# Performance work log

Measured on AMD Instinct MI355X. Metric: run time of the kernel, lower is better.

The kernel has to match this reference:

```python
import jax, jax.numpy as jnp
import numpy as np


def _sq_cdist(a, b):
    # squared Euclidean distances, [N, M]
    a2 = jnp.sum(a * a, axis=1)[:, None]
    b2 = jnp.sum(b * b, axis=1)[None, :]
    d = a2 + b2 - 2.0 * (a @ b.T)
    return jnp.maximum(d, 0.0)


def _gaussian_kernel_mean(a, b, sigmas):
    # mean over N*M of sum_k exp(-dist / (2*sigma_k))
    dist = _sq_cdist(a, b)                      # [N, M]
    beta = 1.0 / (2.0 * sigmas)                 # [K]
    s = jnp.exp(-beta[:, None, None] * dist[None, :, :])  # [K, N, M]
    return jnp.mean(jnp.sum(s, axis=0))


def setup_inputs() -> dict:
    key = jax.random.key(0)
    k1, k2 = jax.random.split(key)
    B, C, H, W = 4, 256, 32, 32
    x = jax.random.normal(k1, (B, C, H, W), dtype=jnp.float32)
    y = jax.random.normal(k2, (B, C, H, W), dtype=jnp.float32)
    sigmas = jnp.array([0.01, 0.1, 1.0, 10.0, 100.0], dtype=jnp.float32)
    return {"x": x, "y": y, "sigmas": sigmas}


def reference(x, y, sigmas):
    B, C, H, W = x.shape
    # (B,C,H,W) -> (B*H*W, C), matching flatten(2).transpose(1,2).reshape(-1,C)
    xf = jnp.transpose(x.reshape(B, C, H * W), (0, 2, 1)).reshape(-1, C)
    yf = jnp.transpose(y.reshape(B, C, H * W), (0, 2, 1)).reshape(-1, C)
    xx = _gaussian_kernel_mean(xf, xf, sigmas)
    yy = _gaussian_kernel_mean(yf, yf, sigmas)
    xy = _gaussian_kernel_mean(xf, yf, sigmas)
    return xx + yy - 2.0 * xy
```

## Files before the change

### kernel.cpp

```cpp
#include <hip/hip_runtime.h>
#include <hip/hip_bf16.h>


#define NSIG 5
#define CKS   262144
#define NBLK2 2080

typedef __attribute__((ext_vector_type(8))) short short8;
typedef __attribute__((ext_vector_type(4))) float floatx4;

__global__ __launch_bounds__(256) void prep_kernel(const float* __restrict__ x,
                                                   const float* __restrict__ y,
                                                   ushort* __restrict__ Zc,
                                                   float* __restrict__ norms) {
    const int bid = blockIdx.x;
    const int t = threadIdx.x;
    const int s = bid >> 8;
    const int b = (bid >> 6) & 3;
    const int p0 = (bid & 63) << 4;
    const float* src = s ? y : x;
    const int n0 = (s << 12) + (b << 10) + p0;

    __shared__ float tile[256][17];

    const int cg = t >> 2;
    const int p4 = (t & 3) << 2;
#pragma unroll
    for (int pass = 0; pass < 4; ++pass) {
        const int c = cg + (pass << 6);
        const float4 v = *(const float4*)(src + (((size_t)((b << 8) + c)) << 10) + p0 + p4);
        tile[c][p4] = v.x; tile[c][p4 + 1] = v.y; tile[c][p4 + 2] = v.z; tile[c][p4 + 3] = v.w;
    }
    __syncthreads();

    const int r = t >> 4;
    const int q = t & 15;
    const int row = n0 + r;
    const int sw = (row >> 1) & 3;
    float nsum = 0.f;
#pragma unroll
    for (int h = 0; h < 2; ++h) {
        const int j = q + (h << 4);
        const int ck = j >> 2;
        const int sq = (j & 3) ^ sw;
        const int c0 = j << 3;
        uint pk[4];
#pragma unroll
        for (int jj = 0; jj < 4; ++jj) {
            const float f0 = tile[c0 + 2 * jj][r];
            const float f1 = tile[c0 + 2 * jj + 1][r];
            const __hip_bfloat16 h0 = __float2bfloat16(f0);
            const __hip_bfloat16 h1 = __float2bfloat16(f1);
            const float q0 = __bfloat162float(h0), q1 = __bfloat162float(h1);
            nsum = fmaf(q0, q0, nsum);
            nsum = fmaf(q1, q1, nsum);
            pk[jj] = (uint)(*(const ushort*)&h0) | ((uint)(*(const ushort*)&h1) << 16);
        }
        *(uint4*)(Zc + (size_t)ck * CKS + (size_t)row * 32 + (sq << 3)) =
            make_uint4(pk[0], pk[1], pk[2], pk[3]);
    }
#pragma unroll
    for (int off = 1; off < 16; off <<= 1) nsum += __shfl_xor(nsum, off, 32);
    if (q == 0) norms[row] = nsum;
}

__global__ __launch_bounds__(256, 3) void gemm_epi(const ushort* __restrict__ Zc,
                                                   const float* __restrict__ norms,
                                                   const float* __restrict__ sigmas,
                                                   float* __restrict__ partials) {
    __shared__ float wsum[4];

    const int t = threadIdx.x;
    const int w = t >> 6, l = t & 63;

    const int lin = blockIdx.x;
    int p = (int)((-4.0f + sqrtf(16.0f + 128.0f * (float)lin)) * (1.0f / 64.0f));
    p = p < 0 ? 0 : (p > 7 ? 7 : p);
    while (p < 7 && 32 * (p + 1) * (p + 1) + 4 * (p + 1) <= lin) ++p;
    while (p > 0 && 32 * p * p + 4 * p > lin) --p;
    const int o = lin - (32 * p * p + 4 * p);
    int c = 7;
#pragma unroll
    for (int cc = 7; cc >= 1; --cc) {
        const int Q = cc * (8 * p + 1) + (cc * (cc - 1)) / 2;
        if (o < Q) c = cc - 1;
    }
    const int Qc = c * (8 * p + 1) + (c * (c - 1)) / 2;
    const int tj2 = 8 * p + c;
    const int ti2 = o - Qc;

    const int ti = (ti2 << 1) + (w >> 1);
    const int tj = (tj2 << 1) + (w & 1);
    const bool active = (ti <= tj);
    const bool diag = (ti == tj);

    const int i0 = ti << 6, j0 = tj << 6;
    const int m = l & 15, q = l >> 4;

    int offA[4], offB[4];
#pragma unroll
    for (int f = 0; f < 4; ++f) {
        const int ra = i0 + (f << 4) + m;
        offA[f] = (ra << 5) + (((q ^ ((ra >> 1) & 3))) << 3);
        const int rb = j0 + (f << 4) + m;
        offB[f] = (rb << 5) + (((q ^ ((rb >> 1) & 3))) << 3);
    }

    floatx4 accf[4][4];
#pragma unroll
    for (int fi = 0; fi < 4; ++fi)
#pragma unroll
        for (int fj = 0; fj < 4; ++fj) accf[fi][fj] = (floatx4){0.f, 0.f, 0.f, 0.f};

    float lsum = 0.f;
    if (active) {
        short8 curA[4], curB[4], nxtA[4], nxtB[4];
#pragma unroll
        for (int f = 0; f < 4; ++f) {
            curA[f] = *(const short8*)(Zc + offA[f]);
            curB[f] = *(const short8*)(Zc + offB[f]);
        }
#pragma unroll
        for (int ck = 0; ck < 8; ++ck) {
            if (ck < 7) {
                const size_t ko = (size_t)(ck + 1) * CKS;
#pragma unroll
                for (int f = 0; f < 4; ++f) {
                    nxtA[f] = *(const short8*)(Zc + ko + offA[f]);
                    nxtB[f] = *(const short8*)(Zc + ko + offB[f]);
                }
            }
#pragma unroll
            for (int fi = 0; fi < 4; ++fi)
#pragma unroll
                for (int fj = 0; fj < 4; ++fj)
                    accf[fi][fj] = __builtin_amdgcn_mfma_f32_16x16x32_bf16(curA[fi], curB[fj], accf[fi][fj], 0, 0, 0);
            if (ck < 7) {
#pragma unroll
                for (int f = 0; f < 4; ++f) { curA[f] = nxtA[f]; curB[f] = nxtB[f]; }
            }
        }

        float c2[NSIG];
#pragma unroll
        for (int k = 0; k < NSIG; ++k) c2[k] = (-0.5f / sigmas[k]) * 1.44269504f;

        const float sgn2 = ((ti < 64) == (tj < 64)) ? 2.f : -2.f;

#pragma unroll
        for (int fi = 0; fi < 4; ++fi) {
            const floatx4 ni4 = *(const floatx4*)(norms + i0 + (fi << 4) + (q << 2));
#pragma unroll
            for (int fj = 0; fj < 4; ++fj) {
                const float njs = norms[j0 + (fj << 4) + m];
#pragma unroll
                for (int v = 0; v < 4; ++v) {
                    float d = fmaf(-2.f, accf[fi][fj][v], ni4[v] + njs);
                    d = fmaxf(d, 0.f);
                    if (diag) {
                        const int dif = ((fi - fj) << 4) + ((q << 2) + v) - m;
                        d = (dif < 0) ? d : 3.0e9f;
                    }
                    accf[fi][fj][v] = d;
                }
            }
        }

        float dmin = accf[0][0][0];
#pragma unroll
        for (int fi = 0; fi < 4; ++fi)
#pragma unroll
            for (int fj = 0; fj < 4; ++fj)
#pragma unroll
                for (int v = 0; v < 4; ++v) dmin = fminf(dmin, accf[fi][fj][v]);
#pragma unroll
        for (int off = 1; off < 64; off <<= 1) dmin = fminf(dmin, __shfl_xor(dmin, off, 64));

#pragma unroll
        for (int k = 0; k < NSIG; ++k) {
            if (c2[k] * dmin >= -126.f) {
#pragma unroll
                for (int fi = 0; fi < 4; ++fi)
#pragma unroll
                    for (int fj = 0; fj < 4; ++fj)
#pragma unroll
                        for (int v = 0; v < 4; ++v)
                            lsum += __builtin_amdgcn_exp2f(c2[k] * accf[fi][fj][v]);
            }
        }
        lsum *= sgn2;
    }

#pragma unroll
    for (int off = 32; off > 0; off >>= 1) lsum += __shfl_down(lsum, off, 64);
    if (l == 0) wsum[w] = lsum;
    __syncthreads();
    if (t == 0) partials[blockIdx.x] = wsum[0] + wsum[1] + wsum[2] + wsum[3];
}

__global__ __launch_bounds__(256) void finalize_kernel(const float* __restrict__ partials,
                                                       float* __restrict__ out) {
    __shared__ double sh[256];
    const int t = threadIdx.x;
    double s = 0.0;
    for (int i = t; i < NBLK2; i += 256) s += (double)partials[i];
    sh[t] = s;
    __syncthreads();
    for (int st = 128; st > 0; st >>= 1) {
        if (t < st) sh[t] += sh[t + st];
        __syncthreads();
    }
    if (t == 0) out[0] = (float)((sh[0] + 8192.0 * NSIG) * (1.0 / (4096.0 * 4096.0)));
}

extern "C" void kernel_launch(void* const* d_in, const int* in_sizes, int n_in,
                              void* d_out, int out_size, void* d_ws, size_t ws_size,
                              hipStream_t stream) {
    const float* x   = (const float*)d_in[0];
    const float* y   = (const float*)d_in[1];
    const float* sig = (const float*)d_in[2];

    ushort* Zc      = (ushort*)d_ws;
    float* norms    = (float*)((char*)d_ws + (size_t)8192 * 256 * 2);
    float* partials = (float*)((char*)norms + 8192 * sizeof(float));
    float* out      = (float*)d_out;

    prep_kernel<<<512, 256, 0, stream>>>(x, y, Zc, norms);
    gemm_epi<<<NBLK2, 256, 0, stream>>>(Zc, norms, sig, partials);
    finalize_kernel<<<1, 256, 0, stream>>>(partials, out);
}
```

Before: 105.1 us.

## Make gemm kernel persistent and prefetch next tile during epilogue

Launches a fixed grid of 694 blocks that loop over the 2080 triangular tile-pairs instead of one block per tile. While the exp epilogue of the current tile runs, the first K-chunk operands and the decode of the next tile are issued, so global-load latency can hide behind the transcendental work. It also hoists the sigma constants and norm loads. The cost is more register pressure under the 3-blocks-per-CU bound and uneven work, since blocks get either 3 or 4 tiles.

```diff
diff --git a/kernel.cpp b/kernel.cpp
--- a/kernel.cpp
+++ b/kernel.cpp
@@ -5,6 +5,7 @@
 #define NSIG 5
 #define CKS   262144
 #define NBLK2 2080
+#define GRIDP 694
 
 typedef __attribute__((ext_vector_type(8))) short short8;
 typedef __attribute__((ext_vector_type(4))) float floatx4;
@@ -64,16 +65,8 @@
     if (q == 0) norms[row] = nsum;
 }
 
-__global__ __launch_bounds__(256, 3) void gemm_epi(const ushort* __restrict__ Zc,
-                                                   const float* __restrict__ norms,
-                                                   const float* __restrict__ sigmas,
-                                                   float* __restrict__ partials) {
-    __shared__ float wsum[4];
-
-    const int t = threadIdx.x;
-    const int w = t >> 6, l = t & 63;
-
-    const int lin = blockIdx.x;
+__device__ __forceinline__ void decode_tile(int lin, int w, int& i0, int& j0,
+                                            bool& active, bool& diag) {
     int p = (int)((-4.0f + sqrtf(16.0f + 128.0f * (float)lin)) * (1.0f / 64.0f));
     p = p < 0 ? 0 : (p > 7 ? 7 : p);
     while (p < 7 && 32 * (p + 1) * (p + 1) + 4 * (p + 1) <= lin) ++p;
@@ -88,38 +81,64 @@
     const int Qc = c * (8 * p + 1) + (c * (c - 1)) / 2;
     const int tj2 = 8 * p + c;
     const int ti2 = o - Qc;
-
     const int ti = (ti2 << 1) + (w >> 1);
     const int tj = (tj2 << 1) + (w & 1);
-    const bool active = (ti <= tj);
-    const bool diag = (ti == tj);
-
-    const int i0 = ti << 6, j0 = tj << 6;
-    const int m = l & 15, q = l >> 4;
-
-    int offA[4], offB[4];
+    active = (ti <= tj);
+    diag = (ti == tj);
+    i0 = ti << 6;
+    j0 = tj << 6;
+}
+
+__device__ __forceinline__ void tile_offsets(int i0, int j0, int m, int q,
+                                             int* offA, int* offB) {
 #pragma unroll
     for (int f = 0; f < 4; ++f) {
         const int ra = i0 + (f << 4) + m;
-        offA[f] = (ra << 5) + (((q ^ ((ra >> 1) & 3))) << 3);
+        offA[f] = (ra << 5) + ((q ^ ((ra >> 1) & 3)) << 3);
         const int rb = j0 + (f << 4) + m;
-        offB[f] = (rb << 5) + (((q ^ ((rb >> 1) & 3))) << 3);
-    }
-
-    floatx4 accf[4][4];
-#pragma unroll
-    for (int fi = 0; fi < 4; ++fi)
-#pragma unroll
-        for (int fj = 0; fj < 4; ++fj) accf[fi][fj] = (floatx4){0.f, 0.f, 0.f, 0.f};
+        offB[f] = (rb << 5) + ((q ^ ((rb >> 1) & 3)) << 3);
+    }
+}
+
+__global__ __launch_bounds__(256, 3) void gemm_epi(const ushort* __restrict__ Zc,
+                                                   const float* __restrict__ norms,
+                                                   const float* __restrict__ sigmas,
+                                                   float* __restrict__ partials) {
+    __shared__ float wsum[4];
+
+    const int t = threadIdx.x;
+    const int w = t >> 6, l = t & 63;
+    const int m = l & 15, q = l >> 4;
+
+    float c2[NSIG];
+#pragma unroll
+    for (int k = 0; k < NSIG; ++k) c2[k] = (-0.5f / sigmas[k]) * 1.44269504f;
+
+    int lin = blockIdx.x;
+    int i0, j0;
+    bool active, diag;
+    decode_tile(lin, w, i0, j0, active, diag);
+    int offA[4], offB[4];
+    tile_offsets(i0, j0, m, q, offA, offB);
+
+    short8 curA[4], curB[4];
+#pragma unroll
+    for (int f = 0; f < 4; ++f) {
+        curA[f] = *(const short8*)(Zc + offA[f]);
+        curB[f] = *(const short8*)(Zc + offB[f]);
+    }
 
     float lsum = 0.f;
-    if (active) {
-        short8 curA[4], curB[4], nxtA[4], nxtB[4];
-#pragma unroll
-        for (int f = 0; f < 4; ++f) {
-            curA[f] = *(const short8*)(Zc + offA[f]);
-            curB[f] = *(const short8*)(Zc + offB[f]);
-        }
+
+#pragma unroll 1
+    for (;;) {
+        floatx4 accf[4][4];
+#pragma unroll
+        for (int fi = 0; fi < 4; ++fi)
+#pragma unroll
+            for (int fj = 0; fj < 4; ++fj) accf[fi][fj] = (floatx4){0.f, 0.f, 0.f, 0.f};
+
+        short8 nxtA[4], nxtB[4];
 #pragma unroll
         for (int ck = 0; ck < 8; ++ck) {
             if (ck < 7) {
@@ -141,54 +160,77 @@
             }
         }
 
-        float c2[NSIG];
-#pragma unroll
-        for (int k = 0; k < NSIG; ++k) c2[k] = (-0.5f / sigmas[k]) * 1.44269504f;
-
-        const float sgn2 = ((ti < 64) == (tj < 64)) ? 2.f : -2.f;
-
-#pragma unroll
-        for (int fi = 0; fi < 4; ++fi) {
-            const floatx4 ni4 = *(const floatx4*)(norms + i0 + (fi << 4) + (q << 2));
-#pragma unroll
-            for (int fj = 0; fj < 4; ++fj) {
-                const float njs = norms[j0 + (fj << 4) + m];
-#pragma unroll
-                for (int v = 0; v < 4; ++v) {
-                    float d = fmaf(-2.f, accf[fi][fj][v], ni4[v] + njs);
-                    d = fmaxf(d, 0.f);
-                    if (diag) {
-                        const int dif = ((fi - fj) << 4) + ((q << 2) + v) - m;
-                        d = (dif < 0) ? d : 3.0e9f;
+        const int ei0 = i0, ej0 = j0;
+        const bool eact = active, ediag = diag;
+        const float esgn2 = ((ei0 < 4096) == (ej0 < 4096)) ? 2.f : -2.f;
+
+        floatx4 ni4[4];
+        float njs[4];
+#pragma unroll
+        for (int fi = 0; fi < 4; ++fi)
+            ni4[fi] = *(const floatx4*)(norms + ei0 + (fi << 4) + (q << 2));
+#pragma unroll
+        for (int fj = 0; fj < 4; ++fj)
+            njs[fj] = norms[ej0 + (fj << 4) + m];
+
+        const int lin2 = lin + GRIDP;
+        const bool have2 = (lin2 < NBLK2);
+        if (have2) {
+            decode_tile(lin2, w, i0, j0, active, diag);
+            tile_offsets(i0, j0, m, q, offA, offB);
+#pragma unroll
+            for (int f = 0; f < 4; ++f) {
+                curA[f] = *(const short8*)(Zc + offA[f]);
+                curB[f] = *(const short8*)(Zc + offB[f]);
+            }
+        }
+
+        if (eact) {
+#pragma unroll
+            for (int fi = 0; fi < 4; ++fi) {
+#pragma unroll
+                for (int fj = 0; fj < 4; ++fj) {
+#pragma unroll
+                    for (int v = 0; v < 4; ++v) {
+                        float d = fmaf(-2.f, accf[fi][fj][v], ni4[fi][v] + njs[fj]);
+                        d = fmaxf(d, 0.f);
+                        if (ediag) {
+                            const int dif = ((fi - fj) << 4) + ((q << 2) + v) - m;
+                            d = (dif < 0) ? d : 3.0e9f;
+                        }
+                        accf[fi][fj][v] = d;
                     }
-                    accf[fi][fj][v] = d;
                 }
             }
-        }
-
-        float dmin = accf[0][0][0];
-#pragma unroll
-        for (int fi = 0; fi < 4; ++fi)
-#pragma unroll
-            for (int fj = 0; fj < 4; ++fj)
-#pragma unroll
-                for (int v = 0; v < 4; ++v) dmin = fminf(dmin, accf[fi][fj][v]);
-#pragma unroll
-        for (int off = 1; off < 64; off <<= 1) dmin = fminf(dmin, __shfl_xor(dmin, off, 64));
-
-#pragma unroll
-        for (int k = 0; k < NSIG; ++k) {
-            if (c2[k] * dmin >= -126.f) {
-#pragma unroll
-                for (int fi = 0; fi < 4; ++fi)
-#pragma unroll
-                    for (int fj = 0; fj < 4; ++fj)
-#pragma unroll
-                        for (int v = 0; v < 4; ++v)
-                            lsum += __builtin_amdgcn_exp2f(c2[k] * accf[fi][fj][v]);
-            }
-        }
-        lsum *= sgn2;
+
+            float dmin = accf[0][0][0];
+#pragma unroll
+            for (int fi = 0; fi < 4; ++fi)
+#pragma unroll
+                for (int fj = 0; fj < 4; ++fj)
+#pragma unroll
+                    for (int v = 0; v < 4; ++v) dmin = fminf(dmin, accf[fi][fj][v]);
+#pragma unroll
+            for (int off = 1; off < 64; off <<= 1) dmin = fminf(dmin, __shfl_xor(dmin, off, 64));
+
+            float tsum = 0.f;
+#pragma unroll
+            for (int k = 0; k < NSIG; ++k) {
+                if (c2[k] * dmin >= -126.f) {
+#pragma unroll
+                    for (int fi = 0; fi < 4; ++fi)
+#pragma unroll
+                        for (int fj = 0; fj < 4; ++fj)
+#pragma unroll
+                            for (int v = 0; v < 4; ++v)
+                                tsum += __builtin_amdgcn_exp2f(c2[k] * accf[fi][fj][v]);
+                }
+            }
+            lsum = fmaf(esgn2, tsum, lsum);
+        }
+
+        lin = lin2;
+        if (!have2) break;
     }
 
 #pragma unroll
@@ -203,7 +245,7 @@
     __shared__ double sh[256];
     const int t = threadIdx.x;
     double s = 0.0;
-    for (int i = t; i < NBLK2; i += 256) s += (double)partials[i];
+    for (int i = t; i < GRIDP; i += 256) s += (double)partials[i];
     sh[t] = s;
     __syncthreads();
     for (int st = 128; st > 0; st >>= 1) {
@@ -226,6 +268,6 @@
     float* out      = (float*)d_out;
 
     prep_kernel<<<512, 256, 0, stream>>>(x, y, Zc, norms);
-    gemm_epi<<<NBLK2, 256, 0, stream>>>(Zc, norms, sig, partials);
+    gemm_epi<<<GRIDP, 256, 0, stream>>>(Zc, norms, sig, partials);
     finalize_kernel<<<1, 256, 0, stream>>>(partials, out);
 }
```

New measurement: 96.67 us. 8.0% less time.

## Enlarge per-wave GEMM tile to 128x64 with two-wave blocks

Applied to the files above, without the earlier changes.

Each block now runs 2 waves instead of 4, and each wave computes a 128x64 distance tile instead of 64x64. The 8 A fragments are shared across 4 B fragments, so fewer global fragment loads are issued per MFMA. Diagonal blocks no longer have an idle wave: both waves compute their full tile, and the lower-triangle masking now takes the wave's column offset into account. The trade-off is a much larger accumulator and prefetch register footprint per wave, with fewer waves per block and possibly lower occupancy to hide load latency.

```diff
diff --git a/kernel.cpp b/kernel.cpp
--- a/kernel.cpp
+++ b/kernel.cpp
@@ -64,14 +64,15 @@
     if (q == 0) norms[row] = nsum;
 }
 
-__global__ __launch_bounds__(256, 3) void gemm_epi(const ushort* __restrict__ Zc,
+__global__ __launch_bounds__(128, 2) void gemm_epi(const ushort* __restrict__ Zc,
                                                    const float* __restrict__ norms,
                                                    const float* __restrict__ sigmas,
                                                    float* __restrict__ partials) {
-    __shared__ float wsum[4];
+    __shared__ float wsum[2];
 
     const int t = threadIdx.x;
     const int w = t >> 6, l = t & 63;
+    const int m = l & 15, q = l >> 4;
 
     const int lin = blockIdx.x;
     int p = (int)((-4.0f + sqrtf(16.0f + 128.0f * (float)lin)) * (1.0f / 64.0f));
@@ -88,114 +89,116 @@
     const int Qc = c * (8 * p + 1) + (c * (c - 1)) / 2;
     const int tj2 = 8 * p + c;
     const int ti2 = o - Qc;
-
-    const int ti = (ti2 << 1) + (w >> 1);
-    const int tj = (tj2 << 1) + (w & 1);
-    const bool active = (ti <= tj);
-    const bool diag = (ti == tj);
-
-    const int i0 = ti << 6, j0 = tj << 6;
-    const int m = l & 15, q = l >> 4;
-
-    int offA[4], offB[4];
+    const bool diag = (ti2 == tj2);
+
+    const int i0 = ti2 << 7;
+    const int jj0 = (tj2 << 7) + (w << 6);
+
+    int offA[8], offB[4];
+#pragma unroll
+    for (int f = 0; f < 8; ++f) {
+        const int ra = i0 + (f << 4) + m;
+        offA[f] = (ra << 5) + ((q ^ ((ra >> 1) & 3)) << 3);
+    }
 #pragma unroll
     for (int f = 0; f < 4; ++f) {
-        const int ra = i0 + (f << 4) + m;
-        offA[f] = (ra << 5) + (((q ^ ((ra >> 1) & 3))) << 3);
-        const int rb = j0 + (f << 4) + m;
-        offB[f] = (rb << 5) + (((q ^ ((rb >> 1) & 3))) << 3);
-    }
-
-    floatx4 accf[4][4];
-#pragma unroll
-    for (int fi = 0; fi < 4; ++fi)
+        const int rb = jj0 + (f << 4) + m;
+        offB[f] = (rb << 5) + ((q ^ ((rb >> 1) & 3)) << 3);
+    }
+
+    floatx4 accf[8][4];
+#pragma unroll
+    for (int fi = 0; fi < 8; ++fi)
 #pragma unroll
         for (int fj = 0; fj < 4; ++fj) accf[fi][fj] = (floatx4){0.f, 0.f, 0.f, 0.f};
 
+    short8 curA[8], curB[4];
+#pragma unroll
+    for (int f = 0; f < 8; ++f) curA[f] = *(const short8*)(Zc + offA[f]);
+#pragma unroll
+    for (int f = 0; f < 4; ++f) curB[f] = *(const short8*)(Zc + offB[f]);
+
+#pragma unroll
+    for (int ck = 0; ck < 8; ++ck) {
+        short8 nxtA[8], nxtB[4];
+        if (ck < 7) {
+            const size_t ko = (size_t)(ck + 1) * CKS;
+#pragma unroll
+            for (int f = 0; f < 8; ++f) nxtA[f] = *(const short8*)(Zc + ko + offA[f]);
+#pragma unroll
+            for (int f = 0; f < 4; ++f) nxtB[f] = *(const short8*)(Zc + ko + offB[f]);
+        }
+#pragma unroll
+        for (int fi = 0; fi < 8; ++fi)
+#pragma unroll
+            for (int fj = 0; fj < 4; ++fj)
+                accf[fi][fj] = __builtin_amdgcn_mfma_f32_16x16x32_bf16(curA[fi], curB[fj], accf[fi][fj], 0, 0, 0);
+        if (ck < 7) {
+#pragma unroll
+            for (int f = 0; f < 8; ++f) curA[f] = nxtA[f];
+#pragma unroll
+            for (int f = 0; f < 4; ++f) curB[f] = nxtB[f];
+        }
+    }
+
+    float c2[NSIG];
+#pragma unroll
+    for (int k = 0; k < NSIG; ++k) c2[k] = (-0.5f / sigmas[k]) * 1.44269504f;
+
+    const float sgn2 = ((i0 < 4096) == (jj0 < 4096)) ? 2.f : -2.f;
+
+    float njs[4];
+#pragma unroll
+    for (int fj = 0; fj < 4; ++fj) njs[fj] = norms[jj0 + (fj << 4) + m];
+
+#pragma unroll
+    for (int fi = 0; fi < 8; ++fi) {
+        const floatx4 ni4 = *(const floatx4*)(norms + i0 + (fi << 4) + (q << 2));
+#pragma unroll
+        for (int fj = 0; fj < 4; ++fj) {
+#pragma unroll
+            for (int v = 0; v < 4; ++v) {
+                float d = fmaf(-2.f, accf[fi][fj][v], ni4[v] + njs[fj]);
+                d = fmaxf(d, 0.f);
+                if (diag) {
+                    const int dif = ((fi - fj) << 4) + ((q << 2) + v) - (w << 6) - m;
+                    d = (dif < 0) ? d : 3.0e9f;
+                }
+                accf[fi][fj][v] = d;
+            }
+        }
+    }
+
+    float dmin = accf[0][0][0];
+#pragma unroll
+    for (int fi = 0; fi < 8; ++fi)
+#pragma unroll
+        for (int fj = 0; fj < 4; ++fj)
+#pragma unroll
+            for (int v = 0; v < 4; ++v) dmin = fminf(dmin, accf[fi][fj][v]);
+#pragma unroll
+    for (int off = 1; off < 64; off <<= 1) dmin = fminf(dmin, __shfl_xor(dmin, off, 64));
+
     float lsum = 0.f;
-    if (active) {
-        short8 curA[4], curB[4], nxtA[4], nxtB[4];
-#pragma unroll
-        for (int f = 0; f < 4; ++f) {
-            curA[f] = *(const short8*)(Zc + offA[f]);
-            curB[f] = *(const short8*)(Zc + offB[f]);
-        }
-#pragma unroll
-        for (int ck = 0; ck < 8; ++ck) {
-            if (ck < 7) {
-                const size_t ko = (size_t)(ck + 1) * CKS;
-#pragma unroll
-                for (int f = 0; f < 4; ++f) {
-                    nxtA[f] = *(const short8*)(Zc + ko + offA[f]);
-                    nxtB[f] = *(const short8*)(Zc + ko + offB[f]);
-                }
-            }
-#pragma unroll
-            for (int fi = 0; fi < 4; ++fi)
+#pragma unroll
+    for (int k = 0; k < NSIG; ++k) {
+        if (c2[k] * dmin >= -126.f) {
+#pragma unroll
+            for (int fi = 0; fi < 8; ++fi)
 #pragma unroll
                 for (int fj = 0; fj < 4; ++fj)
-                    accf[fi][fj] = __builtin_amdgcn_mfma_f32_16x16x32_bf16(curA[fi], curB[fj], accf[fi][fj], 0, 0, 0);
-            if (ck < 7) {
-#pragma unroll
-                for (int f = 0; f < 4; ++f) { curA[f] = nxtA[f]; curB[f] = nxtB[f]; }
-            }
-        }
-
-        float c2[NSIG];
-#pragma unroll
-        for (int k = 0; k < NSIG; ++k) c2[k] = (-0.5f / sigmas[k]) * 1.44269504f;
-
-        const float sgn2 = ((ti < 64) == (tj < 64)) ? 2.f : -2.f;
-
-#pragma unroll
-        for (int fi = 0; fi < 4; ++fi) {
-            const floatx4 ni4 = *(const floatx4*)(norms + i0 + (fi << 4) + (q << 2));
-#pragma unroll
-            for (int fj = 0; fj < 4; ++fj) {
-                const float njs = norms[j0 + (fj << 4) + m];
-#pragma unroll
-                for (int v = 0; v < 4; ++v) {
-                    float d = fmaf(-2.f, accf[fi][fj][v], ni4[v] + njs);
-                    d = fmaxf(d, 0.f);
-                    if (diag) {
-                        const int dif = ((fi - fj) << 4) + ((q << 2) + v) - m;
-                        d = (dif < 0) ? d : 3.0e9f;
-                    }
-                    accf[fi][fj][v] = d;
-                }
-            }
-        }
-
-        float dmin = accf[0][0][0];
-#pragma unroll
-        for (int fi = 0; fi < 4; ++fi)
-#pragma unroll
-            for (int fj = 0; fj < 4; ++fj)
-#pragma unroll
-                for (int v = 0; v < 4; ++v) dmin = fminf(dmin, accf[fi][fj][v]);
-#pragma unroll
-        for (int off = 1; off < 64; off <<= 1) dmin = fminf(dmin, __shfl_xor(dmin, off, 64));
-
-#pragma unroll
-        for (int k = 0; k < NSIG; ++k) {
-            if (c2[k] * dmin >= -126.f) {
-#pragma unroll
-                for (int fi = 0; fi < 4; ++fi)
-#pragma unroll
-                    for (int fj = 0; fj < 4; ++fj)
-#pragma unroll
-                        for (int v = 0; v < 4; ++v)
-                            lsum += __builtin_amdgcn_exp2f(c2[k] * accf[fi][fj][v]);
-            }
-        }
-        lsum *= sgn2;
-    }
+#pragma unroll
+                    for (int v = 0; v < 4; ++v)
+                        lsum += __builtin_amdgcn_exp2f(c2[k] * accf[fi][fj][v]);
+        }
+    }
+    lsum *= sgn2;
 
 #pragma unroll
     for (int off = 32; off > 0; off >>= 1) lsum += __shfl_down(lsum, off, 64);
     if (l == 0) wsum[w] = lsum;
     __syncthreads();
-    if (t == 0) partials[blockIdx.x] = wsum[0] + wsum[1] + wsum[2] + wsum[3];
+    if (t == 0) partials[blockIdx.x] = wsum[0] + wsum[1];
 }
 
 __global__ __launch_bounds__(256) void finalize_kernel(const float* __restrict__ partials,
@@ -226,6 +229,6 @@
     float* out      = (float*)d_out;
 
     prep_kernel<<<512, 256, 0, stream>>>(x, y, Zc, norms);
-    gemm_epi<<<NBLK2, 256, 0, stream>>>(Zc, norms, sig, partials);
+    gemm_epi<<<NBLK2, 128, 0, stream>>>(Zc, norms, sig, partials);
     finalize_kernel<<<1, 256, 0, stream>>>(partials, out);
 }
```

New measurement: 111.9 us. 6.5% more time.

## Stage GEMM operand tiles in LDS via async global_load_lds double buffering

Applied to the files above, without the earlier changes.

Replaces per-wave direct global loads of A/B fragments with block-cooperative global_load_lds copies into double-buffered shared memory. The four waves of a 128x128 supertile now share one A and one B staging load, and diagonal supertiles reuse the A buffer for B. This cuts redundant global traffic and overlaps the next chunk's load with the current MFMAs. In exchange it adds a barrier per chunk, makes inactive waves join the GEMM loop, and lowers the launch-bounds occupancy hint from 3 to 2 blocks per CU.

```diff
diff --git a/kernel.cpp b/kernel.cpp
--- a/kernel.cpp
+++ b/kernel.cpp
@@ -8,6 +8,10 @@
 
 typedef __attribute__((ext_vector_type(8))) short short8;
 typedef __attribute__((ext_vector_type(4))) float floatx4;
+
+#define GLDS16(gp, lp) __builtin_amdgcn_global_load_lds( \
+    (const __attribute__((address_space(1))) void*)(gp),  \
+    (__attribute__((address_space(3))) void*)(lp), 16, 0, 0)
 
 __global__ __launch_bounds__(256) void prep_kernel(const float* __restrict__ x,
                                                    const float* __restrict__ y,
@@ -64,14 +68,17 @@
     if (q == 0) norms[row] = nsum;
 }
 
-__global__ __launch_bounds__(256, 3) void gemm_epi(const ushort* __restrict__ Zc,
+__global__ __launch_bounds__(256, 2) void gemm_epi(const ushort* __restrict__ Zc,
                                                    const float* __restrict__ norms,
                                                    const float* __restrict__ sigmas,
                                                    float* __restrict__ partials) {
+    __shared__ ushort bufA[2][4096];
+    __shared__ ushort bufB[2][4096];
     __shared__ float wsum[4];
 
     const int t = threadIdx.x;
     const int w = t >> 6, l = t & 63;
+    const int m = l & 15, q = l >> 4;
 
     const int lin = blockIdx.x;
     int p = (int)((-4.0f + sqrtf(16.0f + 128.0f * (float)lin)) * (1.0f / 64.0f));
@@ -88,74 +95,95 @@
     const int Qc = c * (8 * p + 1) + (c * (c - 1)) / 2;
     const int tj2 = 8 * p + c;
     const int ti2 = o - Qc;
+    const bool diagST = (ti2 == tj2);
+
+    const int I0 = ti2 << 7;
+    const int J0 = tj2 << 7;
 
     const int ti = (ti2 << 1) + (w >> 1);
     const int tj = (tj2 << 1) + (w & 1);
     const bool active = (ti <= tj);
     const bool diag = (ti == tj);
-
     const int i0 = ti << 6, j0 = tj << 6;
-    const int m = l & 15, q = l >> 4;
-
-    int offA[4], offB[4];
+
+    int loffA[4], loffB[4];
 #pragma unroll
     for (int f = 0; f < 4; ++f) {
-        const int ra = i0 + (f << 4) + m;
-        offA[f] = (ra << 5) + (((q ^ ((ra >> 1) & 3))) << 3);
-        const int rb = j0 + (f << 4) + m;
-        offB[f] = (rb << 5) + (((q ^ ((rb >> 1) & 3))) << 3);
-    }
+        const int ra = ((w >> 1) << 6) + (f << 4) + m;
+        loffA[f] = (ra << 5) + ((q ^ ((ra >> 1) & 3)) << 3);
+        const int rb = ((w & 1) << 6) + (f << 4) + m;
+        loffB[f] = (rb << 5) + ((q ^ ((rb >> 1) & 3)) << 3);
+    }
+
+    const int sg = (w << 10) + (l << 3);
+    const ushort* gA0 = Zc + (size_t)I0 * 32 + sg;
+    const ushort* gB0 = Zc + (size_t)J0 * 32 + sg;
+    ushort* lA = &bufA[0][w << 10];
+    ushort* lB = &bufB[0][w << 10];
+
+    GLDS16(gA0, lA);
+    GLDS16(gA0 + 512, lA + 512);
+    if (!diagST) {
+        GLDS16(gB0, lB);
+        GLDS16(gB0 + 512, lB + 512);
+    }
+    __syncthreads();
 
     floatx4 accf[4][4];
 #pragma unroll
     for (int fi = 0; fi < 4; ++fi)
 #pragma unroll
         for (int fj = 0; fj < 4; ++fj) accf[fi][fj] = (floatx4){0.f, 0.f, 0.f, 0.f};
+
+#pragma unroll
+    for (int ck = 0; ck < 8; ++ck) {
+        const int half = ck & 1;
+        if (ck < 7) {
+            const size_t ko = (size_t)(ck + 1) * CKS;
+            ushort* nA = &bufA[half ^ 1][w << 10];
+            GLDS16(gA0 + ko, nA);
+            GLDS16(gA0 + ko + 512, nA + 512);
+            if (!diagST) {
+                ushort* nB = &bufB[half ^ 1][w << 10];
+                GLDS16(gB0 + ko, nB);
+                GLDS16(gB0 + ko + 512, nB + 512);
+            }
+        }
+        const ushort* rA = &bufA[half][0];
+        const ushort* rB = diagST ? &bufA[half][0] : &bufB[half][0];
+        short8 fa[4], fb[4];
+#pragma unroll
+        for (int f = 0; f < 4; ++f) fa[f] = *(const short8*)(rA + loffA[f]);
+#pragma unroll
+        for (int f = 0; f < 4; ++f) fb[f] = *(const short8*)(rB + loffB[f]);
+#pragma unroll
+        for (int fi = 0; fi < 4; ++fi)
+#pragma unroll
+            for (int fj = 0; fj < 4; ++fj)
+                accf[fi][fj] = __builtin_amdgcn_mfma_f32_16x16x32_bf16(fa[fi], fb[fj], accf[fi][fj], 0, 0, 0);
+        __syncthreads();
+    }
 
     float lsum = 0.f;
     if (active) {
-        short8 curA[4], curB[4], nxtA[4], nxtB[4];
-#pragma unroll
-        for (int f = 0; f < 4; ++f) {
-            curA[f] = *(const short8*)(Zc + offA[f]);
-            curB[f] = *(const short8*)(Zc + offB[f]);
-        }
-#pragma unroll
-        for (int ck = 0; ck < 8; ++ck) {
-            if (ck < 7) {
-                const size_t ko = (size_t)(ck + 1) * CKS;
-#pragma unroll
-                for (int f = 0; f < 4; ++f) {
-                    nxtA[f] = *(const short8*)(Zc + ko + offA[f]);
-                    nxtB[f] = *(const short8*)(Zc + ko + offB[f]);
-                }
-            }
-#pragma unroll
-            for (int fi = 0; fi < 4; ++fi)
-#pragma unroll
-                for (int fj = 0; fj < 4; ++fj)
-                    accf[fi][fj] = __builtin_amdgcn_mfma_f32_16x16x32_bf16(curA[fi], curB[fj], accf[fi][fj], 0, 0, 0);
-            if (ck < 7) {
-#pragma unroll
-                for (int f = 0; f < 4; ++f) { curA[f] = nxtA[f]; curB[f] = nxtB[f]; }
-            }
-        }
-
         float c2[NSIG];
 #pragma unroll
         for (int k = 0; k < NSIG; ++k) c2[k] = (-0.5f / sigmas[k]) * 1.44269504f;
 
-        const float sgn2 = ((ti < 64) == (tj < 64)) ? 2.f : -2.f;
+        const float sgn2 = ((i0 < 4096) == (j0 < 4096)) ? 2.f : -2.f;
+
+        float njs[4];
+#pragma unroll
+        for (int fj = 0; fj < 4; ++fj) njs[fj] = norms[j0 + (fj << 4) + m];
 
 #pragma unroll
         for (int fi = 0; fi < 4; ++fi) {
             const floatx4 ni4 = *(const floatx4*)(norms + i0 + (fi << 4) + (q << 2));
 #pragma unroll
             for (int fj = 0; fj < 4; ++fj) {
-                const float njs = norms[j0 + (fj << 4) + m];
 #pragma unroll
                 for (int v = 0; v < 4; ++v) {
-                    float d = fmaf(-2.f, accf[fi][fj][v], ni4[v] + njs);
+                    float d = fmaf(-2.f, accf[fi][fj][v], ni4[v] + njs[fj]);
                     d = fmaxf(d, 0.f);
                     if (diag) {
                         const int dif = ((fi - fj) << 4) + ((q << 2) + v) - m;
@@ -176,6 +204,7 @@
 #pragma unroll
         for (int off = 1; off < 64; off <<= 1) dmin = fminf(dmin, __shfl_xor(dmin, off, 64));
 
+        float tsum = 0.f;
 #pragma unroll
         for (int k = 0; k < NSIG; ++k) {
             if (c2[k] * dmin >= -126.f) {
@@ -185,10 +214,10 @@
                     for (int fj = 0; fj < 4; ++fj)
 #pragma unroll
                         for (int v = 0; v < 4; ++v)
-                            lsum += __builtin_amdgcn_exp2f(c2[k] * accf[fi][fj][v]);
+                            tsum += __builtin_amdgcn_exp2f(c2[k] * accf[fi][fj][v]);
             }
         }
-        lsum *= sgn2;
+        lsum = sgn2 * tsum;
     }
 
 #pragma unroll
```

Measured after the change: 96.86 us. 1.08x faster.
